# Kernel tuning notes

Measured on AMD Instinct MI355X. Metric: run time of the kernel, lower is better.

Reference implementation:

```python
import jax, jax.numpy as jnp
import numpy as np

D = 3          # matrix dimension (fixed in source)
WIDTH = 23     # hidden channel width (fixed in source)
B = 524288     # batch of 3x3 symmetric matrices

# layer channel dims: {1:1}->{1:W}, W->W, W->W, W->1
_LAYER_DIMS = [(1, WIDTH), (WIDTH, WIDTH), (WIDTH, WIDTH), (WIDTH, 1)]


def setup_inputs() -> dict:
    key = jax.random.key(0)
    ks = jax.random.split(key, 1 + 3 * len(_LAYER_DIMS))
    a = jax.random.normal(ks[0], (B, D, D), dtype=jnp.float32)
    x = a + jnp.swapaxes(a, -1, -2)  # symmetric inputs, as eigh expects
    inp = {"x": x}
    for li, (ic, oc) in enumerate(_LAYER_DIMS):
        s = 1.0 / np.sqrt(2.0 * ic * D)
        inp[f"w_id{li}"] = (jax.random.normal(ks[1 + 3 * li], (oc, ic)) * s).astype(jnp.float32)
        inp[f"w_sum{li}"] = (jax.random.normal(ks[2 + 3 * li], (oc, ic)) * s).astype(jnp.float32)
        inp[f"b{li}"] = jnp.zeros((oc,), dtype=jnp.float32)
    return inp


def _perm_layer(t, w_id, w_sum, b):
    # t: (B, in_c, D). S_D-equivariant linear map on order-1 tensors:
    # identity basis + all-ones(sum) basis + constant-vector bias.
    y = jnp.einsum('oc,bcd->bod', w_id, t)
    y = y + jnp.einsum('oc,bc->bo', w_sum, t.sum(-1))[:, :, None]
    return y + b[None, :, None]


def reference(x, w_id0, w_sum0, b0, w_id1, w_sum1, b1,
              w_id2, w_sum2, b2, w_id3, w_sum3, b3):
    evals, evecs = jnp.linalg.eigh(x)          # (B,D), (B,D,D)
    t = evals[:, None, :]                      # (B,1,D)
    layers = [(w_id0, w_sum0, b0), (w_id1, w_sum1, b1),
              (w_id2, w_sum2, b2), (w_id3, w_sum3, b3)]
    for i, (wi, ws, b) in enumerate(layers):
        t = _perm_layer(t, wi, ws, b)
        if i < len(layers) - 1:
            t = jax.nn.relu(t)
    ev = t[:, 0, :]                            # (B,D) transformed eigenvalues
    # eigvecs @ diag(ev) @ eigvecs^T, batched
    return jnp.einsum('bik,bk,bjk->bij', evecs, ev, evecs)
```

## Files before the change

### kernel.cpp

```cpp
#include <hip/hip_runtime.h>
#include <math.h>


#define MLP_W 23

typedef _Float16 h2    __attribute__((ext_vector_type(2)));
typedef _Float16 f16x4 __attribute__((ext_vector_type(4)));
typedef _Float16 f16x8 __attribute__((ext_vector_type(8)));
typedef float    f32x4 __attribute__((ext_vector_type(4)));

__device__ __attribute__((aligned(16))) h2 g_afrag[2][2][2][64][4];
__device__ __attribute__((aligned(16))) h2 g_a3frag[64][4];

__global__ void svh_prep_kernel(const float* __restrict__ wi1, const float* __restrict__ ws1,
                                const float* __restrict__ wi2, const float* __restrict__ ws2,
                                const float* __restrict__ wi3, const float* __restrict__ ws3) {
    int t = blockIdx.x * blockDim.x + threadIdx.x;
    if (t < 512) {
        int lane  = t & 63;
        int mt    = (t >> 6) & 1;
        int mat   = (t >> 7) & 1;
        int layer = (t >> 8) & 1;
        const float* W = layer ? (mat ? ws2 : wi2) : (mat ? ws1 : wi1);
        int row = mt * 16 + (lane & 15);
        int g   = lane >> 4;
#pragma unroll
        for (int dw = 0; dw < 4; ++dw) {
            int k0 = 8 * g + 2 * dw, k1 = k0 + 1;
            float a = (row < MLP_W && k0 < MLP_W) ? W[row * MLP_W + k0] : 0.0f;
            float b = (row < MLP_W && k1 < MLP_W) ? W[row * MLP_W + k1] : 0.0f;
            g_afrag[layer][mat][mt][lane][dw] = (h2){(_Float16)a, (_Float16)b};
        }
    }
    if (t < 64) {
        int lane = t;
        int row  = lane & 15;
        int g    = lane >> 4;
#pragma unroll
        for (int dw = 0; dw < 4; ++dw) {
            int k0 = 8 * g + 2 * dw, k1 = k0 + 1;
            float a = 0.0f, b = 0.0f;
            if (row == 0) {
                a = (k0 < MLP_W) ? wi3[k0] : 0.0f;
                b = (k1 < MLP_W) ? wi3[k1] : 0.0f;
            } else if (row == 1) {
                a = (k0 < MLP_W) ? ws3[k0] : 0.0f;
                b = (k1 < MLP_W) ? ws3[k1] : 0.0f;
            }
            g_a3frag[lane][dw] = (h2){(_Float16)a, (_Float16)b};
        }
    }
}

__device__ __forceinline__ float sinv(float d) {
    return (fabsf(d) > 1e-20f) ? (1.0f / d) : 0.0f;
}

__device__ __forceinline__ f32x4 mm16(f16x8 a, f16x8 b) {
    return __builtin_amdgcn_mfma_f32_16x16x32_f16(a, b, (f32x4){0.f, 0.f, 0.f, 0.f}, 0, 0, 0);
}
__device__ __forceinline__ f32x4 mm16a(f16x8 a, f16x8 b, f32x4 c) {
    return __builtin_amdgcn_mfma_f32_16x16x32_f16(a, b, c, 0, 0, 0);
}

#define COL_STRIDE 56
#define CHB   (64 * COL_STRIDE)
#define ZOFF  (3 * CHB)
#define LDSZ  (ZOFF + 16)

__global__ __launch_bounds__(64, 4)
void svh_eig_mlp_kernel(
    const float* __restrict__ x,
    const float* __restrict__ wi0, const float* __restrict__ ws0, const float* __restrict__ bb0,
    const float* __restrict__ bb1, const float* __restrict__ bb2, const float* __restrict__ bb3,
    float* __restrict__ out, int B)
{
    __shared__ alignas(16) unsigned char lds[LDSZ];

    const int lane = threadIdx.x;
    const int g    = lane >> 4;
    const int c16  = lane & 15;
    int idx  = blockIdx.x * 64 + lane;
    int cidx = (idx < B) ? idx : (B - 1);

    const float* xp = x + (size_t)cidx * 9;
    float x00 = xp[0], x01 = xp[1], x02 = xp[2];
    float x11 = xp[4], x12 = xp[5], x22 = xp[8];

    if (lane < 2) *(f16x4*)(lds + ZOFF + 8 * lane) = (f16x4){0, 0, 0, 0};

    float q   = (x00 + x11 + x22) * (1.0f / 3.0f);
    float a00 = x00 - q, a11 = x11 - q, a22 = x22 - q;
    float p1  = x01 * x01 + x02 * x02 + x12 * x12;
    float p2  = a00 * a00 + a11 * a11 + a22 * a22 + 2.0f * p1;
    float p   = sqrtf(p2 * (1.0f / 6.0f));
    float ip  = sinv(p);
    float d00 = a00 * ip, d11 = a11 * ip, d22 = a22 * ip;
    float c01 = x01 * ip, c02 = x02 * ip, c12 = x12 * ip;
    float detB = d00 * (d11 * d22 - c12 * c12)
               - c01 * (c01 * d22 - c12 * c02)
               + c02 * (c01 * c12 - d11 * c02);
    float r = 0.5f * detB;
    r = fminf(1.0f, fmaxf(-1.0f, r));
    float phi  = acosf(r) * (1.0f / 3.0f);
    float cph  = __cosf(phi);
    float sph  = sqrtf(fmaxf(0.0f, 1.0f - cph * cph));
    const float SQ3 = 1.7320508075688772f;
    float lc = q + 2.0f * p * cph;
    float la = q - p * cph - SQ3 * p * sph;
    float lb = q - p * cph + SQ3 * p * sph;

    {
        float S = la + lb + lc;
        const int base = lane * COL_STRIDE;
#pragma unroll
        for (int m = 0; m < 6; ++m) {
            float t0[4], t1[4], t2[4];
#pragma unroll
            for (int rr = 0; rr < 4; ++rr) {
                int o = 4 * m + rr;
                if (o < MLP_W) {
                    float wiv = wi0[o];
                    float u   = fmaf(ws0[o], S, bb0[o]);
                    t0[rr] = fmaxf(0.0f, fmaf(wiv, la, u));
                    t1[rr] = fmaxf(0.0f, fmaf(wiv, lb, u));
                    t2[rr] = fmaxf(0.0f, fmaf(wiv, lc, u));
                } else { t0[rr] = t1[rr] = t2[rr] = 0.0f; }
            }
            f16x4 v0 = {(_Float16)t0[0], (_Float16)t0[1], (_Float16)t0[2], (_Float16)t0[3]};
            f16x4 v1 = {(_Float16)t1[0], (_Float16)t1[1], (_Float16)t1[2], (_Float16)t1[3]};
            f16x4 v2 = {(_Float16)t2[0], (_Float16)t2[1], (_Float16)t2[2], (_Float16)t2[3]};
            *(f16x4*)(lds + 0 * CHB + base + 8 * m) = v0;
            *(f16x4*)(lds + 1 * CHB + base + 8 * m) = v1;
            *(f16x4*)(lds + 2 * CHB + base + 8 * m) = v2;
        }
    }

    const f16x8 A3 = *(const f16x8*)(&g_a3frag[lane][0]);

    float eva = 0.0f, evb = 0.0f, evc = 0.0f;

#pragma unroll
    for (int L = 0; L < 2; ++L) {
        f16x8 WiM0 = *(const f16x8*)(&g_afrag[L][0][0][lane][0]);
        f16x8 WiM1 = *(const f16x8*)(&g_afrag[L][0][1][lane][0]);
        f16x8 WsM0 = *(const f16x8*)(&g_afrag[L][1][0][lane][0]);
        f16x8 WsM1 = *(const f16x8*)(&g_afrag[L][1][1][lane][0]);
        const float* bb = L ? bb2 : bb1;
        float breg[2][4];
#pragma unroll
        for (int mt = 0; mt < 2; ++mt)
#pragma unroll
            for (int rr = 0; rr < 4; ++rr) {
                int row = mt * 16 + 4 * g + rr;
                breg[mt][rr] = (row < MLP_W) ? bb[row] : 0.0f;
            }

#pragma unroll
        for (int pp = 0; pp < 4; ++pp) {
            const int colb = (16 * pp + c16) * COL_STRIDE;
            f16x8 bf[3];
#pragma unroll
            for (int h = 0; h < 3; ++h) {
                int off = (g == 3) ? ZOFF : (h * CHB + colb + g * 16);
                f16x4 lo = *(const f16x4*)(lds + off);
                f16x4 hi = *(const f16x4*)(lds + off + 8);
                bf[h] = __builtin_shufflevector(lo, hi, 0, 1, 2, 3, 4, 5, 6, 7);
            }
            f32x4 c0m0 = mm16(WiM0, bf[0]);
            f32x4 c0m1 = mm16(WiM1, bf[0]);
            f32x4 c1m0 = mm16(WiM0, bf[1]);
            f32x4 c1m1 = mm16(WiM1, bf[1]);
            f32x4 c2m0 = mm16(WiM0, bf[2]);
            f32x4 c2m1 = mm16(WiM1, bf[2]);
            f32x4 sm0 = mm16a(WsM0, bf[2], mm16a(WsM0, bf[1], mm16(WsM0, bf[0])));
            f32x4 sm1 = mm16a(WsM1, bf[2], mm16a(WsM1, bf[1], mm16(WsM1, bf[0])));

#pragma unroll
            for (int mt = 0; mt < 2; ++mt) {
                if (mt == 1 && g >= 2) continue;
                f32x4 c0 = (mt == 0) ? c0m0 : c0m1;
                f32x4 c1 = (mt == 0) ? c1m0 : c1m1;
                f32x4 c2 = (mt == 0) ? c2m0 : c2m1;
                f32x4 cs = (mt == 0) ? sm0  : sm1;
                float y0[4], y1[4], y2[4];
#pragma unroll
                for (int rr = 0; rr < 4; ++rr) {
                    float u  = cs[rr] + breg[mt][rr];
                    y0[rr] = fmaxf(0.0f, c0[rr] + u);
                    y1[rr] = fmaxf(0.0f, c1[rr] + u);
                    y2[rr] = fmaxf(0.0f, c2[rr] + u);
                }
                int wb = colb + mt * 32 + 8 * g;
                f16x4 w0 = {(_Float16)y0[0], (_Float16)y0[1], (_Float16)y0[2], (_Float16)y0[3]};
                f16x4 w1 = {(_Float16)y1[0], (_Float16)y1[1], (_Float16)y1[2], (_Float16)y1[3]};
                f16x4 w2 = {(_Float16)y2[0], (_Float16)y2[1], (_Float16)y2[2], (_Float16)y2[3]};
                *(f16x4*)(lds + 0 * CHB + wb) = w0;
                *(f16x4*)(lds + 1 * CHB + wb) = w1;
                *(f16x4*)(lds + 2 * CHB + wb) = w2;
            }

            if (L == 1) {
                f16x8 b2f[3];
#pragma unroll
                for (int h = 0; h < 3; ++h) {
                    int off = (g == 3) ? ZOFF : (h * CHB + colb + g * 16);
                    f16x4 lo = *(const f16x4*)(lds + off);
                    f16x4 hi = *(const f16x4*)(lds + off + 8);
                    b2f[h] = __builtin_shufflevector(lo, hi, 0, 1, 2, 3, 4, 5, 6, 7);
                }
                f32x4 D0 = mm16(A3, b2f[0]);
                f32x4 D1 = mm16(A3, b2f[1]);
                f32x4 D2 = mm16(A3, b2f[2]);
                float ssum = D0[1] + D1[1] + D2[1];
                float ea = D0[0] + ssum;
                float eb = D1[0] + ssum;
                float ec = D2[0] + ssum;
                ea = __shfl(ea, c16);
                eb = __shfl(eb, c16);
                ec = __shfl(ec, c16);
                bool own = (g == pp);
                eva = own ? ea : eva;
                evb = own ? eb : evb;
                evc = own ? ec : evc;
            }
        }
    }

    {
        float b3v = bb3[0];
        eva += b3v; evb += b3v; evc += b3v;
    }

    float g1 = (evb - eva) * sinv(lb - la);
    float g2 = (evc - evb) * sinv(lc - lb);
    float c2 = (g2 - g1) * sinv(lc - la);

    float m100 = x00 - la, m111 = x11 - la, m122 = x22 - la;
    float m200 = x00 - lb, m211 = x11 - lb, m222 = x22 - lb;

    float P00 = m100 * m200 + x01 * x01 + x02 * x02;
    float P01 = m100 * x01 + x01 * m211 + x02 * x12;
    float P02 = m100 * x02 + x01 * x12 + x02 * m222;
    float P11 = x01 * x01 + m111 * m211 + x12 * x12;
    float P12 = x01 * x02 + m111 * x12 + x12 * m222;
    float P22 = x02 * x02 + x12 * x12 + m122 * m222;

    float o00 = fmaf(g1, m100, eva) + c2 * P00;
    float o01 = g1 * x01 + c2 * P01;
    float o02 = g1 * x02 + c2 * P02;
    float o11 = fmaf(g1, m111, eva) + c2 * P11;
    float o12 = g1 * x12 + c2 * P12;
    float o22 = fmaf(g1, m122, eva) + c2 * P22;

    if (idx < B) {
        float* op = out + (size_t)idx * 9;
        op[0] = o00; op[1] = o01; op[2] = o02;
        op[3] = o01; op[4] = o11; op[5] = o12;
        op[6] = o02; op[7] = o12; op[8] = o22;
    }
}

extern "C" void kernel_launch(void* const* d_in, const int* in_sizes, int n_in,
                              void* d_out, int out_size, void* d_ws, size_t ws_size,
                              hipStream_t stream) {
    const float* x   = (const float*)d_in[0];
    const float* wi0 = (const float*)d_in[1];
    const float* ws0 = (const float*)d_in[2];
    const float* b0  = (const float*)d_in[3];
    const float* wi1 = (const float*)d_in[4];
    const float* ws1 = (const float*)d_in[5];
    const float* b1  = (const float*)d_in[6];
    const float* wi2 = (const float*)d_in[7];
    const float* ws2 = (const float*)d_in[8];
    const float* b2  = (const float*)d_in[9];
    const float* wi3 = (const float*)d_in[10];
    const float* ws3 = (const float*)d_in[11];
    const float* b3  = (const float*)d_in[12];

    int B = in_sizes[0] / 9;
    float* out = (float*)d_out;

    {
        dim3 block(256);
        dim3 grid(2);
        hipLaunchKernelGGL(svh_prep_kernel, grid, block, 0, stream,
                           wi1, ws1, wi2, ws2, wi3, ws3);
    }

    dim3 block(64);
    dim3 grid((B + 63) / 64);
    hipLaunchKernelGGL(svh_eig_mlp_kernel, grid, block, 0, stream,
                       x, wi0, ws0, b0, b1, b2, b3,
                       out, B);
}
```

Measured before the change: 119.6 us.

## Interleave LDS activation layout per column and vectorize layer-0 and epilogue math

Reorganizes the LDS activation buffer so each batch column holds the three eigenvalue channels interleaved in 16-byte chunks. MFMA B-fragments can then be read with a single 16-byte LDS load instead of two 8-byte loads. Layer-0 weights are padded into a global buffer by the prep kernel so they can be loaded as float2 and processed with packed FMA/max. The input matrix is loaded with vector loads, and the bias/ReLU epilogue is vectorized. The risk is different LDS bank-conflict patterns from the new 144-byte column stride.

```diff
diff --git a/kernel.cpp b/kernel.cpp
--- a/kernel.cpp
+++ b/kernel.cpp
@@ -8,11 +8,16 @@
 typedef _Float16 f16x4 __attribute__((ext_vector_type(4)));
 typedef _Float16 f16x8 __attribute__((ext_vector_type(8)));
 typedef float    f32x4 __attribute__((ext_vector_type(4)));
+typedef float    v2f   __attribute__((ext_vector_type(2)));
+typedef float    f4a   __attribute__((ext_vector_type(4), aligned(4)));
 
 __device__ __attribute__((aligned(16))) h2 g_afrag[2][2][2][64][4];
 __device__ __attribute__((aligned(16))) h2 g_a3frag[64][4];
-
-__global__ void svh_prep_kernel(const float* __restrict__ wi1, const float* __restrict__ ws1,
+__device__ __attribute__((aligned(16))) float g_l0[3][24];
+
+__global__ void svh_prep_kernel(const float* __restrict__ wi0, const float* __restrict__ ws0,
+                                const float* __restrict__ b0,
+                                const float* __restrict__ wi1, const float* __restrict__ ws1,
                                 const float* __restrict__ wi2, const float* __restrict__ ws2,
                                 const float* __restrict__ wi3, const float* __restrict__ ws3) {
     int t = blockIdx.x * blockDim.x + threadIdx.x;
@@ -50,6 +55,11 @@
             g_a3frag[lane][dw] = (h2){(_Float16)a, (_Float16)b};
         }
     }
+    if (t < 24) {
+        g_l0[0][t] = (t < MLP_W) ? wi0[t] : 0.0f;
+        g_l0[1][t] = (t < MLP_W) ? ws0[t] : 0.0f;
+        g_l0[2][t] = (t < MLP_W) ? b0[t]  : 0.0f;
+    }
 }
 
 __device__ __forceinline__ float sinv(float d) {
@@ -63,15 +73,13 @@
     return __builtin_amdgcn_mfma_f32_16x16x32_f16(a, b, c, 0, 0, 0);
 }
 
-#define COL_STRIDE 56
-#define CHB   (64 * COL_STRIDE)
-#define ZOFF  (3 * CHB)
-#define LDSZ  (ZOFF + 16)
+#define COLB 144
+#define ZOFF (64 * COLB)
+#define LDSZ (ZOFF + 16)
 
 __global__ __launch_bounds__(64, 4)
 void svh_eig_mlp_kernel(
     const float* __restrict__ x,
-    const float* __restrict__ wi0, const float* __restrict__ ws0, const float* __restrict__ bb0,
     const float* __restrict__ bb1, const float* __restrict__ bb2, const float* __restrict__ bb3,
     float* __restrict__ out, int B)
 {
@@ -84,10 +92,13 @@
     int cidx = (idx < B) ? idx : (B - 1);
 
     const float* xp = x + (size_t)cidx * 9;
-    float x00 = xp[0], x01 = xp[1], x02 = xp[2];
-    float x11 = xp[4], x12 = xp[5], x22 = xp[8];
-
-    if (lane < 2) *(f16x4*)(lds + ZOFF + 8 * lane) = (f16x4){0, 0, 0, 0};
+    f4a xa = *(const f4a*)(xp);
+    f4a xb = *(const f4a*)(xp + 4);
+    float x22 = xp[8];
+    float x00 = xa[0], x01 = xa[1], x02 = xa[2];
+    float x11 = xb[0], x12 = xb[1];
+
+    if (lane == 0) *(f32x4*)(lds + ZOFF) = (f32x4){0.f, 0.f, 0.f, 0.f};
 
     float q   = (x00 + x11 + x22) * (1.0f / 3.0f);
     float a00 = x00 - q, a11 = x11 - q, a22 = x22 - q;
@@ -112,33 +123,34 @@
 
     {
         float S = la + lb + lc;
-        const int base = lane * COL_STRIDE;
+        v2f Sv = {S, S}, lav = {la, la}, lbv = {lb, lb}, lcv = {lc, lc};
+        v2f z2 = {0.f, 0.f};
+        const v2f* L0WI = (const v2f*)g_l0[0];
+        const v2f* L0WS = (const v2f*)g_l0[1];
+        const v2f* L0BB = (const v2f*)g_l0[2];
+        const int base = lane * COLB;
 #pragma unroll
         for (int m = 0; m < 6; ++m) {
-            float t0[4], t1[4], t2[4];
-#pragma unroll
-            for (int rr = 0; rr < 4; ++rr) {
-                int o = 4 * m + rr;
-                if (o < MLP_W) {
-                    float wiv = wi0[o];
-                    float u   = fmaf(ws0[o], S, bb0[o]);
-                    t0[rr] = fmaxf(0.0f, fmaf(wiv, la, u));
-                    t1[rr] = fmaxf(0.0f, fmaf(wiv, lb, u));
-                    t2[rr] = fmaxf(0.0f, fmaf(wiv, lc, u));
-                } else { t0[rr] = t1[rr] = t2[rr] = 0.0f; }
-            }
-            f16x4 v0 = {(_Float16)t0[0], (_Float16)t0[1], (_Float16)t0[2], (_Float16)t0[3]};
-            f16x4 v1 = {(_Float16)t1[0], (_Float16)t1[1], (_Float16)t1[2], (_Float16)t1[3]};
-            f16x4 v2 = {(_Float16)t2[0], (_Float16)t2[1], (_Float16)t2[2], (_Float16)t2[3]};
-            *(f16x4*)(lds + 0 * CHB + base + 8 * m) = v0;
-            *(f16x4*)(lds + 1 * CHB + base + 8 * m) = v1;
-            *(f16x4*)(lds + 2 * CHB + base + 8 * m) = v2;
+            v2f wiA = L0WI[2 * m], wiB = L0WI[2 * m + 1];
+            v2f uA  = __builtin_elementwise_fma(L0WS[2 * m],     Sv, L0BB[2 * m]);
+            v2f uB  = __builtin_elementwise_fma(L0WS[2 * m + 1], Sv, L0BB[2 * m + 1]);
+            v2f a0 = __builtin_elementwise_max(__builtin_elementwise_fma(wiA, lav, uA), z2);
+            v2f b0 = __builtin_elementwise_max(__builtin_elementwise_fma(wiB, lav, uB), z2);
+            v2f a1 = __builtin_elementwise_max(__builtin_elementwise_fma(wiA, lbv, uA), z2);
+            v2f b1 = __builtin_elementwise_max(__builtin_elementwise_fma(wiB, lbv, uB), z2);
+            v2f a2 = __builtin_elementwise_max(__builtin_elementwise_fma(wiA, lcv, uA), z2);
+            v2f b2 = __builtin_elementwise_max(__builtin_elementwise_fma(wiB, lcv, uB), z2);
+            int cb = base + (m >> 1) * 48 + (m & 1) * 8;
+            *(f16x4*)(lds + cb +  0) = (f16x4){(_Float16)a0.x, (_Float16)a0.y, (_Float16)b0.x, (_Float16)b0.y};
+            *(f16x4*)(lds + cb + 16) = (f16x4){(_Float16)a1.x, (_Float16)a1.y, (_Float16)b1.x, (_Float16)b1.y};
+            *(f16x4*)(lds + cb + 32) = (f16x4){(_Float16)a2.x, (_Float16)a2.y, (_Float16)b2.x, (_Float16)b2.y};
         }
     }
 
     const f16x8 A3 = *(const f16x8*)(&g_a3frag[lane][0]);
 
     float eva = 0.0f, evb = 0.0f, evc = 0.0f;
+    const f32x4 z4 = {0.f, 0.f, 0.f, 0.f};
 
 #pragma unroll
     for (int L = 0; L < 2; ++L) {
@@ -147,25 +159,23 @@
         f16x8 WsM0 = *(const f16x8*)(&g_afrag[L][1][0][lane][0]);
         f16x8 WsM1 = *(const f16x8*)(&g_afrag[L][1][1][lane][0]);
         const float* bb = L ? bb2 : bb1;
-        float breg[2][4];
+        f32x4 bvec[2];
 #pragma unroll
         for (int mt = 0; mt < 2; ++mt)
 #pragma unroll
             for (int rr = 0; rr < 4; ++rr) {
                 int row = mt * 16 + 4 * g + rr;
-                breg[mt][rr] = (row < MLP_W) ? bb[row] : 0.0f;
+                bvec[mt][rr] = (row < MLP_W) ? bb[row] : 0.0f;
             }
 
 #pragma unroll
         for (int pp = 0; pp < 4; ++pp) {
-            const int colb = (16 * pp + c16) * COL_STRIDE;
+            const int colb = (16 * pp + c16) * COLB;
             f16x8 bf[3];
 #pragma unroll
             for (int h = 0; h < 3; ++h) {
-                int off = (g == 3) ? ZOFF : (h * CHB + colb + g * 16);
-                f16x4 lo = *(const f16x4*)(lds + off);
-                f16x4 hi = *(const f16x4*)(lds + off + 8);
-                bf[h] = __builtin_shufflevector(lo, hi, 0, 1, 2, 3, 4, 5, 6, 7);
+                int off = (g == 3) ? ZOFF : (colb + g * 48 + h * 16);
+                bf[h] = *(const f16x8*)(lds + off);
             }
             f32x4 c0m0 = mm16(WiM0, bf[0]);
             f32x4 c0m1 = mm16(WiM1, bf[0]);
@@ -183,31 +193,22 @@
                 f32x4 c1 = (mt == 0) ? c1m0 : c1m1;
                 f32x4 c2 = (mt == 0) ? c2m0 : c2m1;
                 f32x4 cs = (mt == 0) ? sm0  : sm1;
-                float y0[4], y1[4], y2[4];
-#pragma unroll
-                for (int rr = 0; rr < 4; ++rr) {
-                    float u  = cs[rr] + breg[mt][rr];
-                    y0[rr] = fmaxf(0.0f, c0[rr] + u);
-                    y1[rr] = fmaxf(0.0f, c1[rr] + u);
-                    y2[rr] = fmaxf(0.0f, c2[rr] + u);
-                }
-                int wb = colb + mt * 32 + 8 * g;
-                f16x4 w0 = {(_Float16)y0[0], (_Float16)y0[1], (_Float16)y0[2], (_Float16)y0[3]};
-                f16x4 w1 = {(_Float16)y1[0], (_Float16)y1[1], (_Float16)y1[2], (_Float16)y1[3]};
-                f16x4 w2 = {(_Float16)y2[0], (_Float16)y2[1], (_Float16)y2[2], (_Float16)y2[3]};
-                *(f16x4*)(lds + 0 * CHB + wb) = w0;
-                *(f16x4*)(lds + 1 * CHB + wb) = w1;
-                *(f16x4*)(lds + 2 * CHB + wb) = w2;
+                f32x4 u  = cs + bvec[mt];
+                f32x4 y0 = __builtin_elementwise_max(c0 + u, z4);
+                f32x4 y1 = __builtin_elementwise_max(c1 + u, z4);
+                f32x4 y2 = __builtin_elementwise_max(c2 + u, z4);
+                int wb = colb + (2 * mt + (g >> 1)) * 48 + (g & 1) * 8;
+                *(f16x4*)(lds + wb +  0) = (f16x4){(_Float16)y0[0], (_Float16)y0[1], (_Float16)y0[2], (_Float16)y0[3]};
+                *(f16x4*)(lds + wb + 16) = (f16x4){(_Float16)y1[0], (_Float16)y1[1], (_Float16)y1[2], (_Float16)y1[3]};
+                *(f16x4*)(lds + wb + 32) = (f16x4){(_Float16)y2[0], (_Float16)y2[1], (_Float16)y2[2], (_Float16)y2[3]};
             }
 
             if (L == 1) {
                 f16x8 b2f[3];
 #pragma unroll
                 for (int h = 0; h < 3; ++h) {
-                    int off = (g == 3) ? ZOFF : (h * CHB + colb + g * 16);
-                    f16x4 lo = *(const f16x4*)(lds + off);
-                    f16x4 hi = *(const f16x4*)(lds + off + 8);
-                    b2f[h] = __builtin_shufflevector(lo, hi, 0, 1, 2, 3, 4, 5, 6, 7);
+                    int off = (g == 3) ? ZOFF : (colb + g * 48 + h * 16);
+                    b2f[h] = *(const f16x8*)(lds + off);
                 }
                 f32x4 D0 = mm16(A3, b2f[0]);
                 f32x4 D1 = mm16(A3, b2f[1]);
@@ -285,12 +286,11 @@
         dim3 block(256);
         dim3 grid(2);
         hipLaunchKernelGGL(svh_prep_kernel, grid, block, 0, stream,
-                           wi1, ws1, wi2, ws2, wi3, ws3);
+                           wi0, ws0, b0, wi1, ws1, wi2, ws2, wi3, ws3);
     }
 
     dim3 block(64);
     dim3 grid((B + 63) / 64);
     hipLaunchKernelGGL(svh_eig_mlp_kernel, grid, block, 0, stream,
-                       x, wi0, ws0, b0, b1, b2, b3,
-                       out, B);
-}
+                       x, b1, b2, b3, out, B);
+}
```

Measured after the change: 117.0 us. 2.2% less time.
